# Performance work log

Hardware: AMD Instinct MI355X
Metric: run time of the kernel (lower is better)

Reference implementation:

```python
import jax, jax.numpy as jnp
import numpy as np

ALPHA = 0.25
GAMMA = 2.0
EPS = 1e-4
AREA_THR = 100.0  # 10*10


def calc_iou(a, b):
    # a: anchors [A,4] in (y1,x1,y2,x2); b: boxes [M,4] in (x1,y1,x2,y2)
    area = (b[:, 2] - b[:, 0]) * (b[:, 3] - b[:, 1])  # [M]
    iw = jnp.minimum(a[:, 3:4], b[None, :, 2]) - jnp.maximum(a[:, 1:2], b[None, :, 0])
    ih = jnp.minimum(a[:, 2:3], b[None, :, 3]) - jnp.maximum(a[:, 0:1], b[None, :, 1])
    iw = jnp.clip(iw, 0.0)
    ih = jnp.clip(ih, 0.0)
    ua = (a[:, 2] - a[:, 0])[:, None] * (a[:, 3] - a[:, 1])[:, None] + area[None, :] - iw * ih
    ua = jnp.clip(ua, 1e-8)
    return iw * ih / ua  # [A,M]


def setup_inputs() -> dict:
    key = jax.random.key(0)
    k1, k2, k3, k4, k5, k6, k7 = jax.random.split(key, 7)
    B, M, A, C = 8, 64, 49104, 80
    # GT boxes (x1,y1,x2,y2), well-formed
    xy = jax.random.uniform(k1, (B, M, 2), minval=0.0, maxval=400.0)
    wh = jax.random.uniform(k2, (B, M, 2), minval=10.0, maxval=100.0)
    boxes = jnp.concatenate([xy, xy + wh], axis=-1)
    labels = jax.random.randint(k3, (B, M), 0, C + 1)  # 0 = ignore
    # anchors (y1,x1,y2,x2), well-formed
    ac = jax.random.uniform(k4, (A, 2), minval=0.0, maxval=512.0)
    ahw = jax.random.uniform(k5, (A, 2), minval=16.0, maxval=128.0)
    anchors = jnp.concatenate([ac - 0.5 * ahw, ac + 0.5 * ahw], axis=-1)[None]  # [1,A,4]
    classification = jax.random.uniform(k6, (B, A, C), minval=0.0, maxval=1.0)
    regression = jax.random.normal(k7, (B, A, 4), dtype=jnp.float32)
    return {"boxes": boxes, "labels": labels, "anchors": anchors,
            "classification": classification, "regression": regression}


def _per_image(cls_j, reg_j, box_j, lab_j, anc, aw, ah, acx, acy):
    C = cls_j.shape[-1]
    valid = lab_j != 0  # [M]
    cls = jnp.clip(cls_j, EPS, 1.0 - EPS)
    iou = calc_iou(anc, box_j)                      # [A,M]
    iou = jnp.where(valid[None, :], iou, -1.0)      # mask padded GT
    iou_max = iou.max(axis=1)                       # [A]
    iou_arg = iou.argmax(axis=1)                    # [A]
    ab = box_j[iou_arg]                             # [A,4] assigned boxes
    al = lab_j[iou_arg] - 1                         # [A] assigned labels
    big = (ab[:, 2] - ab[:, 0]) * (ab[:, 3] - ab[:, 1]) > AREA_THR
    pos = (big & (iou_max >= 0.5)) | (~big & (iou_max >= 0.15))  # [A]
    npos = pos.sum().astype(cls.dtype)
    targets = jax.nn.one_hot(al, C, dtype=cls.dtype) * pos[:, None].astype(cls.dtype)
    is_one = targets == 1.0
    alpha_f = jnp.where(is_one, ALPHA, 1.0 - ALPHA)
    focal_w = alpha_f * jnp.where(is_one, 1.0 - cls, cls) ** GAMMA
    bce = -(targets * jnp.log(cls) + (1.0 - targets) * jnp.log(1.0 - cls))
    cls_loss = (focal_w * bce).sum() / jnp.maximum(npos, 1.0)
    gw = ab[:, 2] - ab[:, 0]
    gh = ab[:, 3] - ab[:, 1]
    gcx = ab[:, 0] + 0.5 * gw
    gcy = ab[:, 1] + 0.5 * gh
    gw = jnp.clip(gw, 1.0)
    gh = jnp.clip(gh, 1.0)
    t = jnp.stack([(gcy - acy) / ah, (gcx - acx) / aw,
                   jnp.log(gh / ah), jnp.log(gw / aw)], axis=1)  # [A,4] (dy,dx,dh,dw)
    diff = jnp.abs(t - reg_j)
    rl = jnp.where(diff <= 1.0 / 9.0, 0.5 * 9.0 * diff ** 2, diff - 0.5 / 9.0)
    reg_sum = (rl * pos[:, None].astype(cls.dtype)).sum()
    reg_loss = jnp.where(npos > 0, reg_sum / (4.0 * jnp.maximum(npos, 1.0)), 0.0)
    return cls_loss, reg_loss


def reference(boxes, labels, anchors, classification, regression):
    anc = anchors[0]  # [A,4] (y1,x1,y2,x2)
    aw = anc[:, 3] - anc[:, 1]
    ah = anc[:, 2] - anc[:, 0]
    acx = anc[:, 1] + 0.5 * aw
    acy = anc[:, 0] + 0.5 * ah
    cls_l, reg_l = jax.vmap(_per_image, in_axes=(0, 0, 0, 0, None, None, None, None, None))(
        classification, regression, boxes, labels, anc, aw, ah, acx, acy)
    cls_loss = cls_l.mean(keepdims=True)
    det_loss = reg_l.mean(keepdims=True) * 50.0
    return cls_loss, det_loss
```

## Files before the change

kernel.cpp:

```cpp
#include <hip/hip_runtime.h>

#define NB 8
#define NM 64
#define NA 49104
#define NC 80
#define EPSF 1e-4f
#define BPI 256
#define APB 192

struct Ws {
    float cnp[NB][BPI];
    float regp[NB][BPI];
    float npp[NB][BPI];
};

__device__ __forceinline__ float waveReduceSumF(float v) {
    #pragma unroll
    for (int off = 32; off > 0; off >>= 1) v += __shfl_down(v, off, 64);
    return v;
}

#define NEG_SCALE (-0.51986038542f)

#define CONSUME4(V)                                                   \
    s0 = fmaf((V).x * (V).x, __log2f(fmaxf(1.0f - (V).x, EPSF)), s0); \
    s1 = fmaf((V).y * (V).y, __log2f(fmaxf(1.0f - (V).y, EPSF)), s1); \
    s2 = fmaf((V).z * (V).z, __log2f(fmaxf(1.0f - (V).z, EPSF)), s2); \
    s3 = fmaf((V).w * (V).w, __log2f(fmaxf(1.0f - (V).w, EPSF)), s3);

__device__ __forceinline__ float negConsume(const float4* __restrict__ base,
                                            int b, float4 nv0, float4 nv1) {
    const int per4 = NA * NC / 4;
    const int stride = BPI * 256;
    float s0 = 0.0f, s1 = 0.0f, s2 = 0.0f, s3 = 0.0f;
    float4 v = nv0, vn = nv1;
    #pragma unroll
    for (int k = 0; k < 14; ++k) {
        float4 nx;
        if (k < 12) nx = base[b + (k + 2) * stride];
        CONSUME4(v);
        v = vn; vn = nx;
    }
    if (b < per4 - 14 * stride) {
        float4 vt = base[b + 14 * stride];
        CONSUME4(vt);
    }
    return (s0 + s1) + (s2 + s3);
}

__device__ __forceinline__ void anchorWork(int j, int a, float4 an,
                                           const float4* __restrict__ boxes4,
                                           const int* __restrict__ labels,
                                           const float* __restrict__ cls,
                                           const float4* __restrict__ reg,
                                           float& corr, float& regl, float& npf) {
    const int jb = j * NM;
    const float ay1 = an.x, ax1 = an.y, ay2 = an.z, ax2 = an.w;
    const float aare = (ay2 - ay1) * (ax2 - ax1);

    float best = -1.0f;
    int bi = 0;
    #pragma unroll 16
    for (int m = 0; m < NM; ++m) {
        const float4 bm = boxes4[jb + m];
        const int lab = labels[jb + m];
        const float bar = (bm.z - bm.x) * (bm.w - bm.y);
        const float bar_eff = (lab != 0) ? bar : __builtin_inff();
        float iw = fmaxf(fminf(ax2, bm.z) - fmaxf(ax1, bm.x), 0.0f);
        float ih = fmaxf(fminf(ay2, bm.w) - fmaxf(ay1, bm.y), 0.0f);
        float inter = iw * ih;
        float ua = (aare + bar_eff) - inter;
        float iou = inter * __builtin_amdgcn_rcpf(ua);
        bool upd = iou > best;
        best = upd ? iou : best;
        bi   = upd ? m : bi;
    }

    float4 bb = boxes4[jb + bi];
    int labg = labels[jb + bi];
    const float bar = (bb.z - bb.x) * (bb.w - bb.y);
    const bool big = bar > 100.0f;
    const float thr = big ? 0.5f : 0.15f;
    const bool pos = best >= thr;
    if (pos) {
        npf = 1.0f;
        const int al = labg - 1;
        float p = cls[((size_t)j * NA + a) * NC + al];
        p = fminf(fmaxf(p, EPSF), 1.0f - EPSF);
        const float om = 1.0f - p;
        corr = 0.25f * om * om * (-__logf(p)) - 0.75f * p * p * (-__logf(om));

        const float aw = ax2 - ax1, ah = ay2 - ay1;
        const float acx = ax1 + 0.5f * aw, acy = ay1 + 0.5f * ah;
        float gw = bb.z - bb.x;
        float gh = bb.w - bb.y;
        const float gcx = bb.x + 0.5f * gw;
        const float gcy = bb.y + 0.5f * gh;
        gw = fmaxf(gw, 1.0f);
        gh = fmaxf(gh, 1.0f);
        float4 r = reg[(size_t)j * NA + a];
        const float t0 = (gcy - acy) / ah;
        const float t1 = (gcx - acx) / aw;
        const float t2 = __logf(gh / ah);
        const float t3 = __logf(gw / aw);
        const float d0 = fabsf(t0 - r.x);
        const float d1 = fabsf(t1 - r.y);
        const float d2 = fabsf(t2 - r.z);
        const float d3 = fabsf(t3 - r.w);
        const float ninth = 1.0f / 9.0f;
        const float c = 0.5f / 9.0f;
        regl  = (d0 <= ninth) ? 4.5f * d0 * d0 : d0 - c;
        regl += (d1 <= ninth) ? 4.5f * d1 * d1 : d1 - c;
        regl += (d2 <= ninth) ? 4.5f * d2 * d2 : d2 - c;
        regl += (d3 <= ninth) ? 4.5f * d3 * d3 : d3 - c;
    }
}

__global__ void main_kernel(const float4* __restrict__ cls4,
                            const float* __restrict__ cls,
                            const float4* __restrict__ anchors4,
                            const float4* __restrict__ reg,
                            const float4* __restrict__ boxes4,
                            const int* __restrict__ labels,
                            Ws* __restrict__ ws) {
    const int j = blockIdx.y;
    const int bx = blockIdx.x;
    const int tid = threadIdx.x;

    const int per4 = NA * NC / 4;
    const int stride = BPI * 256;
    const float4* base = cls4 + (size_t)j * per4;
    const int b = bx * 256 + tid;
    const int a = bx * APB + tid;
    const int ai = a < NA ? a : NA - 1;
    const bool doA = (tid < APB) && (a < NA);

    float corr = 0.0f, regl = 0.0f, npf = 0.0f;
    float S;

    if ((bx & 1) == 0) {
        float4 an = anchors4[ai];
        float4 nv0 = base[b];
        float4 nv1 = base[b + stride];
        if (doA) anchorWork(j, a, an, boxes4, labels, cls, reg, corr, regl, npf);
        S = negConsume(base, b, nv0, nv1);
    } else {
        float4 nv0 = base[b];
        float4 nv1 = base[b + stride];
        S = negConsume(base, b, nv0, nv1);
        float4 an = anchors4[ai];
        if (doA) anchorWork(j, a, an, boxes4, labels, cls, reg, corr, regl, npf);
    }
    float cn = fmaf(NEG_SCALE, S, corr);

    __shared__ float sred[3][4];
    cn   = waveReduceSumF(cn);
    regl = waveReduceSumF(regl);
    npf  = waveReduceSumF(npf);
    const int wid = tid >> 6;
    if ((tid & 63) == 0) {
        sred[0][wid] = cn; sred[1][wid] = regl; sred[2][wid] = npf;
    }
    __syncthreads();
    if (tid == 0) {
        ws->cnp[j][bx]  = sred[0][0] + sred[0][1] + sred[0][2] + sred[0][3];
        ws->regp[j][bx] = sred[1][0] + sred[1][1] + sred[1][2] + sred[1][3];
        ws->npp[j][bx]  = sred[2][0] + sred[2][1] + sred[2][2] + sred[2][3];
    }
}

__global__ void finalize_kernel(const Ws* __restrict__ ws, float* __restrict__ out) {
    __shared__ float scls[NB], sreg[NB];
    const int w = threadIdx.x >> 6;
    const int lane = threadIdx.x & 63;
    float cs = 0.0f, rs = 0.0f, np = 0.0f;
    #pragma unroll
    for (int i = lane; i < BPI; i += 64) {
        cs += ws->cnp[w][i];
        rs += ws->regp[w][i];
        np += ws->npp[w][i];
    }
    cs = waveReduceSumF(cs);
    rs = waveReduceSumF(rs);
    np = waveReduceSumF(np);
    if (lane == 0) {
        float d = fmaxf(np, 1.0f);
        scls[w] = cs / d;
        sreg[w] = (np > 0.0f) ? rs / (4.0f * d) : 0.0f;
    }
    __syncthreads();
    if (threadIdx.x == 0) {
        float acc = 0.0f, bsum = 0.0f;
        #pragma unroll
        for (int jj = 0; jj < NB; ++jj) { acc += scls[jj]; bsum += sreg[jj]; }
        out[0] = acc / (float)NB;
        out[1] = (bsum / (float)NB) * 50.0f;
    }
}

extern "C" void kernel_launch(void* const* d_in, const int* in_sizes, int n_in,
                              void* d_out, int out_size, void* d_ws, size_t ws_size,
                              hipStream_t stream) {
    const float* boxes   = (const float*)d_in[0];
    const int*   labels  = (const int*)d_in[1];
    const float* anchors = (const float*)d_in[2];
    const float* cls     = (const float*)d_in[3];
    const float* reg     = (const float*)d_in[4];
    float* out = (float*)d_out;
    Ws* ws = (Ws*)d_ws;

    dim3 g(BPI, NB);
    main_kernel<<<g, 256, 0, stream>>>((const float4*)cls, cls,
                                       (const float4*)anchors, (const float4*)reg,
                                       (const float4*)boxes, labels, ws);

    finalize_kernel<<<1, 512, 0, stream>>>(ws, out);
}
```

Measured before the change: 38.25 us.

## Concentrate anchor IoU matching in first wave with three anchors per lane

```diff
diff --git a/kernel.cpp b/kernel.cpp
--- a/kernel.cpp
+++ b/kernel.cpp
@@ -48,74 +48,6 @@
     return (s0 + s1) + (s2 + s3);
 }
 
-__device__ __forceinline__ void anchorWork(int j, int a, float4 an,
-                                           const float4* __restrict__ boxes4,
-                                           const int* __restrict__ labels,
-                                           const float* __restrict__ cls,
-                                           const float4* __restrict__ reg,
-                                           float& corr, float& regl, float& npf) {
-    const int jb = j * NM;
-    const float ay1 = an.x, ax1 = an.y, ay2 = an.z, ax2 = an.w;
-    const float aare = (ay2 - ay1) * (ax2 - ax1);
-
-    float best = -1.0f;
-    int bi = 0;
-    #pragma unroll 16
-    for (int m = 0; m < NM; ++m) {
-        const float4 bm = boxes4[jb + m];
-        const int lab = labels[jb + m];
-        const float bar = (bm.z - bm.x) * (bm.w - bm.y);
-        const float bar_eff = (lab != 0) ? bar : __builtin_inff();
-        float iw = fmaxf(fminf(ax2, bm.z) - fmaxf(ax1, bm.x), 0.0f);
-        float ih = fmaxf(fminf(ay2, bm.w) - fmaxf(ay1, bm.y), 0.0f);
-        float inter = iw * ih;
-        float ua = (aare + bar_eff) - inter;
-        float iou = inter * __builtin_amdgcn_rcpf(ua);
-        bool upd = iou > best;
-        best = upd ? iou : best;
-        bi   = upd ? m : bi;
-    }
-
-    float4 bb = boxes4[jb + bi];
-    int labg = labels[jb + bi];
-    const float bar = (bb.z - bb.x) * (bb.w - bb.y);
-    const bool big = bar > 100.0f;
-    const float thr = big ? 0.5f : 0.15f;
-    const bool pos = best >= thr;
-    if (pos) {
-        npf = 1.0f;
-        const int al = labg - 1;
-        float p = cls[((size_t)j * NA + a) * NC + al];
-        p = fminf(fmaxf(p, EPSF), 1.0f - EPSF);
-        const float om = 1.0f - p;
-        corr = 0.25f * om * om * (-__logf(p)) - 0.75f * p * p * (-__logf(om));
-
-        const float aw = ax2 - ax1, ah = ay2 - ay1;
-        const float acx = ax1 + 0.5f * aw, acy = ay1 + 0.5f * ah;
-        float gw = bb.z - bb.x;
-        float gh = bb.w - bb.y;
-        const float gcx = bb.x + 0.5f * gw;
-        const float gcy = bb.y + 0.5f * gh;
-        gw = fmaxf(gw, 1.0f);
-        gh = fmaxf(gh, 1.0f);
-        float4 r = reg[(size_t)j * NA + a];
-        const float t0 = (gcy - acy) / ah;
-        const float t1 = (gcx - acx) / aw;
-        const float t2 = __logf(gh / ah);
-        const float t3 = __logf(gw / aw);
-        const float d0 = fabsf(t0 - r.x);
-        const float d1 = fabsf(t1 - r.y);
-        const float d2 = fabsf(t2 - r.z);
-        const float d3 = fabsf(t3 - r.w);
-        const float ninth = 1.0f / 9.0f;
-        const float c = 0.5f / 9.0f;
-        regl  = (d0 <= ninth) ? 4.5f * d0 * d0 : d0 - c;
-        regl += (d1 <= ninth) ? 4.5f * d1 * d1 : d1 - c;
-        regl += (d2 <= ninth) ? 4.5f * d2 * d2 : d2 - c;
-        regl += (d3 <= ninth) ? 4.5f * d3 * d3 : d3 - c;
-    }
-}
-
 __global__ void main_kernel(const float4* __restrict__ cls4,
                             const float* __restrict__ cls,
                             const float4* __restrict__ anchors4,
@@ -131,26 +63,90 @@
     const int stride = BPI * 256;
     const float4* base = cls4 + (size_t)j * per4;
     const int b = bx * 256 + tid;
-    const int a = bx * APB + tid;
-    const int ai = a < NA ? a : NA - 1;
-    const bool doA = (tid < APB) && (a < NA);
+    const int jb = j * NM;
 
     float corr = 0.0f, regl = 0.0f, npf = 0.0f;
-    float S;
-
-    if ((bx & 1) == 0) {
-        float4 an = anchors4[ai];
-        float4 nv0 = base[b];
-        float4 nv1 = base[b + stride];
-        if (doA) anchorWork(j, a, an, boxes4, labels, cls, reg, corr, regl, npf);
-        S = negConsume(base, b, nv0, nv1);
+    float4 nv0, nv1;
+
+    if (tid < 64) {
+        int aq[3];  bool av[3];
+        float ax1[3], ay1[3], ax2[3], ay2[3], aare[3], best[3];
+        int bi[3];
+        #pragma unroll
+        for (int q = 0; q < 3; ++q) {
+            aq[q] = bx * APB + q * 64 + tid;
+            av[q] = aq[q] < NA;
+            float4 an = anchors4[av[q] ? aq[q] : NA - 1];
+            ay1[q] = an.x; ax1[q] = an.y; ay2[q] = an.z; ax2[q] = an.w;
+            aare[q] = (an.z - an.x) * (an.w - an.y);
+            best[q] = -1.0f; bi[q] = 0;
+        }
+        nv0 = base[b];
+        nv1 = base[b + stride];
+
+        #pragma unroll 8
+        for (int m = 0; m < NM; ++m) {
+            const float4 bm = boxes4[jb + m];
+            const int lab = labels[jb + m];
+            const float bar = (bm.z - bm.x) * (bm.w - bm.y);
+            const float bar_eff = (lab != 0) ? bar : __builtin_inff();
+            #pragma unroll
+            for (int q = 0; q < 3; ++q) {
+                float iw = fmaxf(fminf(ax2[q], bm.z) - fmaxf(ax1[q], bm.x), 0.0f);
+                float ih = fmaxf(fminf(ay2[q], bm.w) - fmaxf(ay1[q], bm.y), 0.0f);
+                float inter = iw * ih;
+                float ua = (aare[q] + bar_eff) - inter;
+                float iou = inter * __builtin_amdgcn_rcpf(ua);
+                bool upd = iou > best[q];
+                best[q] = upd ? iou : best[q];
+                bi[q]   = upd ? m : bi[q];
+            }
+        }
+
+        #pragma unroll
+        for (int q = 0; q < 3; ++q) {
+            if (!av[q]) continue;
+            float4 bb = boxes4[jb + bi[q]];
+            int labg = labels[jb + bi[q]];
+            const float bar = (bb.z - bb.x) * (bb.w - bb.y);
+            const float thr = (bar > 100.0f) ? 0.5f : 0.15f;
+            if (best[q] >= thr) {
+                npf += 1.0f;
+                const int al = labg - 1;
+                float p = cls[((size_t)j * NA + aq[q]) * NC + al];
+                p = fminf(fmaxf(p, EPSF), 1.0f - EPSF);
+                const float om = 1.0f - p;
+                corr += 0.25f * om * om * (-__logf(p)) - 0.75f * p * p * (-__logf(om));
+
+                const float aw = ax2[q] - ax1[q], ah = ay2[q] - ay1[q];
+                const float acx = ax1[q] + 0.5f * aw, acy = ay1[q] + 0.5f * ah;
+                float gw = bb.z - bb.x, gh = bb.w - bb.y;
+                const float gcx = bb.x + 0.5f * gw, gcy = bb.y + 0.5f * gh;
+                gw = fmaxf(gw, 1.0f);
+                gh = fmaxf(gh, 1.0f);
+                float4 r = reg[(size_t)j * NA + aq[q]];
+                const float t0 = (gcy - acy) / ah;
+                const float t1 = (gcx - acx) / aw;
+                const float t2 = __logf(gh / ah);
+                const float t3 = __logf(gw / aw);
+                const float d0 = fabsf(t0 - r.x);
+                const float d1 = fabsf(t1 - r.y);
+                const float d2 = fabsf(t2 - r.z);
+                const float d3 = fabsf(t3 - r.w);
+                const float ninth = 1.0f / 9.0f;
+                const float c = 0.5f / 9.0f;
+                regl += (d0 <= ninth) ? 4.5f * d0 * d0 : d0 - c;
+                regl += (d1 <= ninth) ? 4.5f * d1 * d1 : d1 - c;
+                regl += (d2 <= ninth) ? 4.5f * d2 * d2 : d2 - c;
+                regl += (d3 <= ninth) ? 4.5f * d3 * d3 : d3 - c;
+            }
+        }
     } else {
-        float4 nv0 = base[b];
-        float4 nv1 = base[b + stride];
-        S = negConsume(base, b, nv0, nv1);
-        float4 an = anchors4[ai];
-        if (doA) anchorWork(j, a, an, boxes4, labels, cls, reg, corr, regl, npf);
-    }
+        nv0 = base[b];
+        nv1 = base[b + stride];
+    }
+
+    float S = negConsume(base, b, nv0, nv1);
     float cn = fmaf(NEG_SCALE, S, corr);
 
     __shared__ float sred[3][4];
```

Result: slower. 47.44 us (+24.0%).
